# Kernel tuning notes

Hardware: AMD Instinct MI355X
Metric: run time of the kernel (lower is better)

## Reference

```python
import jax, jax.numpy as jnp
import numpy as np

N, HW, L = 16, 3136, 64
C_IN, C_OUT, D = 256, 512, 256


def setup_inputs() -> dict:
    key = jax.random.key(0)
    ks = jax.random.split(key, 8)
    # xavier-normal-ish scale for weights
    def xav(k, shape):
        fan_in, fan_out = shape[1], shape[0]
        std = (2.0 / (fan_in + fan_out)) ** 0.5
        return jax.random.normal(k, shape, dtype=jnp.float32) * std
    return {
        "x": jax.random.normal(ks[0], (N, HW, C_IN), dtype=jnp.float32),
        "t": jax.random.normal(ks[1], (N, L, D), dtype=jnp.float32),
        "W1": xav(ks[2], (D, C_IN)),      # linear1 weight (out,in), no bias
        "W2": xav(ks[3], (D, D)),         # linear2 weight, no bias
        "W3": xav(ks[4], (C_OUT, D)),     # linear3 weight
        "b3": jnp.zeros((C_OUT,), dtype=jnp.float32),
        "Wd": xav(ks[5], (C_OUT, C_IN)),  # downsample weight
        "bd": jnp.zeros((C_OUT,), dtype=jnp.float32),
    }


def reference(x, t, W1, W2, W3, b3, Wd, bd):
    # x: (N, HW, C_in), t: (N, L, D)
    x_q = jnp.einsum("npc,dc->npd", x, W1)          # (N, HW, D)
    t_q = jnp.einsum("nld,ed->nle", t, W2)          # (N, L, D)
    a = jnp.einsum("npd,nld->npl", x_q, t_q)        # unscaled QK^T (N, HW, L)
    a = jax.nn.softmax(a, axis=2)
    t3 = jnp.einsum("nld,od->nlo", t, W3) + b3      # (N, L, C_out)
    av = jnp.einsum("npl,nlo->npo", a, t3)          # (N, HW, C_out)
    x_ds = jnp.einsum("npc,oc->npo", x, Wd) + bd    # downsample residual
    return x_ds + av
```

## Files before the change

### kernel.cpp

```cpp
#include <hip/hip_runtime.h>


typedef unsigned short u16;
using half8 = __attribute__((ext_vector_type(8))) _Float16;
using f32x4 = __attribute__((ext_vector_type(4))) float;

__device__ __forceinline__ u16 f2h(float f) {
  _Float16 h = (_Float16)f;
  union { _Float16 h; u16 u; } cv; cv.h = h;
  return cv.u;
}

__device__ __forceinline__ f32x4 mfma16(half8 a, half8 b, f32x4 c) {
  return __builtin_amdgcn_mfma_f32_16x16x32_f16(a, b, c, 0, 0, 0);
}

__global__ __launch_bounds__(256) void reblock_kernel(
    const float* __restrict__ W1, const float* __restrict__ W2,
    const float* __restrict__ W3, const float* __restrict__ Wd,
    const float* __restrict__ t,
    u16* __restrict__ W1f, u16* __restrict__ W2f, u16* __restrict__ W3f,
    u16* __restrict__ Wdf, u16* __restrict__ tf) {
  int b = blockIdx.x, k = threadIdx.x;
  const float* src; u16* dst; int row;
  if (b < 256)       { src = W1; dst = W1f; row = b; }
  else if (b < 512)  { src = W2; dst = W2f; row = b - 256; }
  else if (b < 1024) { src = W3; dst = W3f; row = b - 512; }
  else if (b < 1536) { src = Wd; dst = Wdf; row = b - 1024; }
  else               { src = t;  dst = tf;  row = b - 1536; }
  float v = src[(size_t)row*256 + k];
  int flat = ((row >> 4)*8 + (k >> 5))*512 + ((k >> 3) & 3)*128 + (row & 15)*8 + (k & 7);
  dst[flat] = f2h(v);
}

__global__ __launch_bounds__(256) void tq_t3t_kernel(
    const u16* __restrict__ tf, const u16* __restrict__ W2f,
    const u16* __restrict__ W3f, const float* __restrict__ b3,
    u16* __restrict__ tqf, u16* __restrict__ t3f) {
  const int tid = threadIdx.x, w = tid >> 6, lane = tid & 63;
  const int quad = lane >> 4, l16 = lane & 15;
  const int b = blockIdx.x;

  if (b < 64) {
    const int n = b >> 2, eb = b & 3;
    const int gW2 = eb*4 + w;
    f32x4 acc[4];
    #pragma unroll
    for (int mt = 0; mt < 4; ++mt) acc[mt] = (f32x4){0.f, 0.f, 0.f, 0.f};
    #pragma unroll
    for (int kc = 0; kc < 8; ++kc) {
      half8 bf = *(const half8*)(W2f + (gW2*8 + kc)*512 + lane*8);
      #pragma unroll
      for (int mt = 0; mt < 4; ++mt) {
        half8 a = *(const half8*)(tf + ((n*4 + mt)*8 + kc)*512 + lane*8);
        acc[mt] = mfma16(a, bf, acc[mt]);
      }
    }
    #pragma unroll
    for (int mt = 0; mt < 4; ++mt)
      #pragma unroll
      for (int r = 0; r < 4; ++r) {
        int flat = ((n*4 + mt)*8 + eb*2 + (w >> 1))*512
                 + ((w & 1)*2 + (l16 >> 3))*128 + (quad*4 + r)*8 + (l16 & 7);
        tqf[flat] = f2h(acc[mt][r]);
      }
  } else {
    const int b2 = b - 64;
    const int n = b2 >> 3, ob = b2 & 7;
    const int gW3 = ob*4 + w;
    f32x4 acc[4];
    #pragma unroll
    for (int nt = 0; nt < 4; ++nt) acc[nt] = (f32x4){0.f, 0.f, 0.f, 0.f};
    #pragma unroll
    for (int kc = 0; kc < 8; ++kc) {
      half8 a = *(const half8*)(W3f + (gW3*8 + kc)*512 + lane*8);
      #pragma unroll
      for (int nt = 0; nt < 4; ++nt) {
        half8 bf = *(const half8*)(tf + ((n*4 + nt)*8 + kc)*512 + lane*8);
        acc[nt] = mfma16(a, bf, acc[nt]);
      }
    }
    #pragma unroll
    for (int nt = 0; nt < 4; ++nt)
      #pragma unroll
      for (int r = 0; r < 4; ++r) {
        int o = ob*64 + w*16 + quad*4 + r;
        int flat = ((n*32 + ob*4 + w)*2 + (nt >> 1))*512
                 + ((nt & 1)*2 + (l16 >> 3))*128 + (quad*4 + r)*8 + (l16 & 7);
        t3f[flat] = f2h(acc[nt][r] + b3[o]);
      }
  }
}

__global__ __launch_bounds__(512, 4) void main_kernel(
    const float* __restrict__ x, const u16* __restrict__ W1f,
    const u16* __restrict__ Wdf, const u16* __restrict__ tqf,
    const u16* __restrict__ t3f, const float* __restrict__ bd,
    float* __restrict__ out) {
  __shared__ u16 xs[64*264];
  __shared__ __align__(16) u16 pool[64*136];

  const int bid = blockIdx.x;
  const int n = bid / 49;
  const int pt = bid - n*49;
  const int m0 = pt * 64;
  const int tid = threadIdx.x, w = tid >> 6, lane = tid & 63;
  const int quad = lane >> 4, l16 = lane & 15;

  float bias[4];
  #pragma unroll
  for (int ot = 0; ot < 4; ++ot) bias[ot] = bd[w*64 + ot*16 + l16];

  {
    const float4* xg = (const float4*)(x + (size_t)(n*3136 + m0)*256);
    #pragma unroll
    for (int it = 0; it < 8; ++it) {
      int idx = it*512 + tid;
      int r = idx >> 6, c4 = idx & 63;
      float4 v = xg[idx];
      ushort4 u;
      u.x = f2h(v.x); u.y = f2h(v.y); u.z = f2h(v.z); u.w = f2h(v.w);
      *(ushort4*)(&xs[r*264 + c4*4]) = u;
    }
  }
  __syncthreads();

  f32x4 acc2[4];
  #pragma unroll
  for (int lt = 0; lt < 4; ++lt) acc2[lt] = (f32x4){0.f, 0.f, 0.f, 0.f};

  #pragma unroll
  for (int h = 0; h < 2; ++h) {
    f32x4 acc1[4];
    #pragma unroll
    for (int mt = 0; mt < 4; ++mt) acc1[mt] = (f32x4){0.f, 0.f, 0.f, 0.f};

    const u16* w1p = W1f + (h*8 + w)*8*512;
    #pragma unroll
    for (int kc = 0; kc < 8; ++kc) {
      half8 bf = *(const half8*)(w1p + kc*512 + lane*8);
      #pragma unroll
      for (int mt = 0; mt < 4; ++mt) {
        half8 a = *(const half8*)(&xs[(mt*16 + l16)*264 + kc*32 + quad*8]);
        acc1[mt] = mfma16(a, bf, acc1[mt]);
      }
    }
    __syncthreads();
    #pragma unroll
    for (int mt = 0; mt < 4; ++mt)
      #pragma unroll
      for (int r = 0; r < 4; ++r)
        pool[(mt*16 + quad*4 + r)*136 + w*16 + l16] = f2h(acc1[mt][r]);
    __syncthreads();

    if (w < 4) {
      #pragma unroll
      for (int k2 = 0; k2 < 4; ++k2) {
        half8 a = *(const half8*)(&pool[(w*16 + l16)*136 + k2*32 + quad*8]);
        #pragma unroll
        for (int lt = 0; lt < 4; ++lt) {
          half8 bf = *(const half8*)(tqf + ((n*4 + lt)*8 + h*4 + k2)*512 + lane*8);
          acc2[lt] = mfma16(a, bf, acc2[lt]);
        }
      }
    }
  }
  __syncthreads();

  if (w < 4) {
    #pragma unroll
    for (int r = 0; r < 4; ++r) {
      float s0 = acc2[0][r], s1 = acc2[1][r], s2 = acc2[2][r], s3 = acc2[3][r];
      float mx = fmaxf(fmaxf(s0, s1), fmaxf(s2, s3));
      #pragma unroll
      for (int off = 8; off >= 1; off >>= 1) mx = fmaxf(mx, __shfl_xor(mx, off, 64));
      float e0 = __expf(s0 - mx), e1 = __expf(s1 - mx);
      float e2 = __expf(s2 - mx), e3 = __expf(s3 - mx);
      float s = e0 + e1 + e2 + e3;
      #pragma unroll
      for (int off = 8; off >= 1; off >>= 1) s += __shfl_xor(s, off, 64);
      float inv = 1.0f / s;
      int row = (w*16 + quad*4 + r)*72;
      pool[row +  0 + l16] = f2h(e0 * inv);
      pool[row + 16 + l16] = f2h(e1 * inv);
      pool[row + 32 + l16] = f2h(e2 * inv);
      pool[row + 48 + l16] = f2h(e3 * inv);
    }
  }
  __syncthreads();

  f32x4 acc[4][4];
  #pragma unroll
  for (int mt = 0; mt < 4; ++mt)
    #pragma unroll
    for (int ot = 0; ot < 4; ++ot) acc[mt][ot] = (f32x4){0.f, 0.f, 0.f, 0.f};

  #pragma unroll
  for (int kc3 = 0; kc3 < 2; ++kc3) {
    half8 a[4];
    #pragma unroll
    for (int mt = 0; mt < 4; ++mt)
      a[mt] = *(const half8*)(&pool[(mt*16 + l16)*72 + kc3*32 + quad*8]);
    #pragma unroll
    for (int ot = 0; ot < 4; ++ot) {
      half8 bf = *(const half8*)(t3f + ((n*32 + w*4 + ot)*2 + kc3)*512 + lane*8);
      #pragma unroll
      for (int mt = 0; mt < 4; ++mt) acc[mt][ot] = mfma16(a[mt], bf, acc[mt][ot]);
    }
  }
  #pragma unroll
  for (int kc = 0; kc < 8; ++kc) {
    half8 a[4];
    #pragma unroll
    for (int mt = 0; mt < 4; ++mt)
      a[mt] = *(const half8*)(&xs[(mt*16 + l16)*264 + kc*32 + quad*8]);
    #pragma unroll
    for (int ot = 0; ot < 4; ++ot) {
      half8 bf = *(const half8*)(Wdf + ((w*4 + ot)*8 + kc)*512 + lane*8);
      #pragma unroll
      for (int mt = 0; mt < 4; ++mt) acc[mt][ot] = mfma16(a[mt], bf, acc[mt][ot]);
    }
  }
  __syncthreads();

  float* pf = (float*)pool;
  #pragma unroll
  for (int c = 0; c < 8; ++c) {
    int mt = c >> 1;
    if ((quad >> 1) == (c & 1)) {
      int rl = (quad & 1)*4;
      #pragma unroll
      for (int ot = 0; ot < 4; ++ot)
        #pragma unroll
        for (int r = 0; r < 4; ++r)
          pf[(rl + r)*520 + w*64 + ot*16 + l16] = acc[mt][ot][r] + bias[ot];
    }
    __syncthreads();
    #pragma unroll
    for (int j = 0; j < 2; ++j) {
      int flat = j*512 + tid;
      int rl = flat >> 7, c4 = (flat & 127)*4;
      float4 v = *(float4*)&pf[rl*520 + c4];
      *(float4*)&out[(size_t)(n*3136 + m0 + c*8 + rl)*512 + c4] = v;
    }
    __syncthreads();
  }
}

extern "C" void kernel_launch(void* const* d_in, const int* in_sizes, int n_in,
                              void* d_out, int out_size, void* d_ws, size_t ws_size,
                              hipStream_t stream) {
  const float* x  = (const float*)d_in[0];
  const float* t  = (const float*)d_in[1];
  const float* W1 = (const float*)d_in[2];
  const float* W2 = (const float*)d_in[3];
  const float* W3 = (const float*)d_in[4];
  const float* b3 = (const float*)d_in[5];
  const float* Wd = (const float*)d_in[6];
  const float* bd = (const float*)d_in[7];
  float* out = (float*)d_out;

  char* ws = (char*)d_ws;
  u16* W1f = (u16*)(ws + 0);
  u16* W2f = (u16*)(ws + 131072);
  u16* W3f = (u16*)(ws + 262144);
  u16* Wdf = (u16*)(ws + 524288);
  u16* tf  = (u16*)(ws + 786432);
  u16* tqf = (u16*)(ws + 1310720);
  u16* t3f = (u16*)(ws + 1835008);

  hipLaunchKernelGGL(reblock_kernel, dim3(2560), dim3(256), 0, stream,
                     W1, W2, W3, Wd, t, W1f, W2f, W3f, Wdf, tf);
  hipLaunchKernelGGL(tq_t3t_kernel, dim3(192), dim3(256), 0, stream,
                     tf, W2f, W3f, b3, tqf, t3f);
  hipLaunchKernelGGL(main_kernel, dim3(784), dim3(512), 0, stream,
                     x, W1f, Wdf, tqf, t3f, bd, out);
}
```

Before: 200.4 us.

## Overlap attention stages with downsample GEMM and use per-wave output staging

The fused kernel's schedule is reordered. W1 fragments for the first half are prefetched into registers before the x tile loads. The second-half x·W1 GEMM is interleaved with the first-half QK^T product, and the downsample GEMM now runs before the softmax barrier so its MFMAs can hide synchronisation latency. The epilogue replaces the block-wide eight-step staged store, which had two barriers per step, with a barrier-free per-wave staging area carved from a unified shared-memory buffer. The cost is higher register pressure from the prefetched W1 fragments and from the output accumulators staying live longer, which could limit occupancy.

New measurement: 196.8 us. Within noise of the previous version (-1.8%).

```diff
diff --git a/kernel.cpp b/kernel.cpp
--- a/kernel.cpp
+++ b/kernel.cpp
@@ -97,8 +97,9 @@
     const u16* __restrict__ Wdf, const u16* __restrict__ tqf,
     const u16* __restrict__ t3f, const float* __restrict__ bd,
     float* __restrict__ out) {
-  __shared__ u16 xs[64*264];
-  __shared__ __align__(16) u16 pool[64*136];
+  __shared__ __attribute__((aligned(16))) char smem[34816 + 17408];
+  u16* xs   = (u16*)smem;
+  u16* pool = (u16*)(smem + 34816);
 
   const int bid = blockIdx.x;
   const int n = bid / 49;
@@ -107,6 +108,12 @@
   const int tid = threadIdx.x, w = tid >> 6, lane = tid & 63;
   const int quad = lane >> 4, l16 = lane & 15;
 
+  half8 w1a[8];
+  {
+    const u16* p = W1f + (size_t)w*8*512;
+    #pragma unroll
+    for (int kc = 0; kc < 8; ++kc) w1a[kc] = *(const half8*)(p + kc*512 + lane*8);
+  }
   float bias[4];
   #pragma unroll
   for (int ot = 0; ot < 4; ++ot) bias[ot] = bd[w*64 + ot*16 + l16];
@@ -125,44 +132,88 @@
   }
   __syncthreads();
 
+  f32x4 acc1[4];
+  #pragma unroll
+  for (int mt = 0; mt < 4; ++mt) acc1[mt] = (f32x4){0.f, 0.f, 0.f, 0.f};
+  #pragma unroll
+  for (int kc = 0; kc < 8; ++kc)
+    #pragma unroll
+    for (int mt = 0; mt < 4; ++mt) {
+      half8 a = *(const half8*)(&xs[(mt*16 + l16)*264 + kc*32 + quad*8]);
+      acc1[mt] = mfma16(a, w1a[kc], acc1[mt]);
+    }
+  #pragma unroll
+  for (int mt = 0; mt < 4; ++mt)
+    #pragma unroll
+    for (int r = 0; r < 4; ++r)
+      pool[(mt*16 + quad*4 + r)*136 + w*16 + l16] = f2h(acc1[mt][r]);
+  __syncthreads();
+
   f32x4 acc2[4];
   #pragma unroll
   for (int lt = 0; lt < 4; ++lt) acc2[lt] = (f32x4){0.f, 0.f, 0.f, 0.f};
-
-  #pragma unroll
-  for (int h = 0; h < 2; ++h) {
-    f32x4 acc1[4];
-    #pragma unroll
-    for (int mt = 0; mt < 4; ++mt) acc1[mt] = (f32x4){0.f, 0.f, 0.f, 0.f};
-
-    const u16* w1p = W1f + (h*8 + w)*8*512;
+  f32x4 acc[4][4];
+  #pragma unroll
+  for (int mt = 0; mt < 4; ++mt)
+    #pragma unroll
+    for (int ot = 0; ot < 4; ++ot) acc[mt][ot] = (f32x4){0.f, 0.f, 0.f, 0.f};
+
+  f32x4 acc1b[4];
+  #pragma unroll
+  for (int mt = 0; mt < 4; ++mt) acc1b[mt] = (f32x4){0.f, 0.f, 0.f, 0.f};
+  {
+    const u16* p = W1f + (size_t)(8 + w)*8*512;
     #pragma unroll
     for (int kc = 0; kc < 8; ++kc) {
-      half8 bf = *(const half8*)(w1p + kc*512 + lane*8);
+      half8 bf = *(const half8*)(p + kc*512 + lane*8);
       #pragma unroll
       for (int mt = 0; mt < 4; ++mt) {
         half8 a = *(const half8*)(&xs[(mt*16 + l16)*264 + kc*32 + quad*8]);
-        acc1[mt] = mfma16(a, bf, acc1[mt]);
-      }
-    }
-    __syncthreads();
+        acc1b[mt] = mfma16(a, bf, acc1b[mt]);
+      }
+    }
+  }
+  if (w < 4) {
+    #pragma unroll
+    for (int k2 = 0; k2 < 4; ++k2) {
+      half8 a = *(const half8*)(&pool[(w*16 + l16)*136 + k2*32 + quad*8]);
+      #pragma unroll
+      for (int lt = 0; lt < 4; ++lt) {
+        half8 bf = *(const half8*)(tqf + ((n*4 + lt)*8 + 0*4 + k2)*512 + lane*8);
+        acc2[lt] = mfma16(a, bf, acc2[lt]);
+      }
+    }
+  }
+  __syncthreads();
+  #pragma unroll
+  for (int mt = 0; mt < 4; ++mt)
+    #pragma unroll
+    for (int r = 0; r < 4; ++r)
+      pool[(mt*16 + quad*4 + r)*136 + w*16 + l16] = f2h(acc1b[mt][r]);
+  __syncthreads();
+
+  if (w < 4) {
+    #pragma unroll
+    for (int k2 = 0; k2 < 4; ++k2) {
+      half8 a = *(const half8*)(&pool[(w*16 + l16)*136 + k2*32 + quad*8]);
+      #pragma unroll
+      for (int lt = 0; lt < 4; ++lt) {
+        half8 bf = *(const half8*)(tqf + ((n*4 + lt)*8 + 1*4 + k2)*512 + lane*8);
+        acc2[lt] = mfma16(a, bf, acc2[lt]);
+      }
+    }
+  }
+  #pragma unroll
+  for (int kc = 0; kc < 8; ++kc) {
+    half8 a[4];
     #pragma unroll
     for (int mt = 0; mt < 4; ++mt)
-      #pragma unroll
-      for (int r = 0; r < 4; ++r)
-        pool[(mt*16 + quad*4 + r)*136 + w*16 + l16] = f2h(acc1[mt][r]);
-    __syncthreads();
-
-    if (w < 4) {
-      #pragma unroll
-      for (int k2 = 0; k2 < 4; ++k2) {
-        half8 a = *(const half8*)(&pool[(w*16 + l16)*136 + k2*32 + quad*8]);
-        #pragma unroll
-        for (int lt = 0; lt < 4; ++lt) {
-          half8 bf = *(const half8*)(tqf + ((n*4 + lt)*8 + h*4 + k2)*512 + lane*8);
-          acc2[lt] = mfma16(a, bf, acc2[lt]);
-        }
-      }
+      a[mt] = *(const half8*)(&xs[(mt*16 + l16)*264 + kc*32 + quad*8]);
+    #pragma unroll
+    for (int ot = 0; ot < 4; ++ot) {
+      half8 bf = *(const half8*)(Wdf + ((w*4 + ot)*8 + kc)*512 + lane*8);
+      #pragma unroll
+      for (int mt = 0; mt < 4; ++mt) acc[mt][ot] = mfma16(a[mt], bf, acc[mt][ot]);
     }
   }
   __syncthreads();
@@ -189,12 +240,6 @@
   }
   __syncthreads();
 
-  f32x4 acc[4][4];
-  #pragma unroll
-  for (int mt = 0; mt < 4; ++mt)
-    #pragma unroll
-    for (int ot = 0; ot < 4; ++ot) acc[mt][ot] = (f32x4){0.f, 0.f, 0.f, 0.f};
-
   #pragma unroll
   for (int kc3 = 0; kc3 < 2; ++kc3) {
     half8 a[4];
@@ -208,42 +253,20 @@
       for (int mt = 0; mt < 4; ++mt) acc[mt][ot] = mfma16(a[mt], bf, acc[mt][ot]);
     }
   }
-  #pragma unroll
-  for (int kc = 0; kc < 8; ++kc) {
-    half8 a[4];
-    #pragma unroll
-    for (int mt = 0; mt < 4; ++mt)
-      a[mt] = *(const half8*)(&xs[(mt*16 + l16)*264 + kc*32 + quad*8]);
-    #pragma unroll
-    for (int ot = 0; ot < 4; ++ot) {
-      half8 bf = *(const half8*)(Wdf + ((w*4 + ot)*8 + kc)*512 + lane*8);
-      #pragma unroll
-      for (int mt = 0; mt < 4; ++mt) acc[mt][ot] = mfma16(a[mt], bf, acc[mt][ot]);
-    }
-  }
-  __syncthreads();
-
-  float* pf = (float*)pool;
-  #pragma unroll
-  for (int c = 0; c < 8; ++c) {
-    int mt = c >> 1;
-    if ((quad >> 1) == (c & 1)) {
-      int rl = (quad & 1)*4;
-      #pragma unroll
-      for (int ot = 0; ot < 4; ++ot)
-        #pragma unroll
-        for (int r = 0; r < 4; ++r)
-          pf[(rl + r)*520 + w*64 + ot*16 + l16] = acc[mt][ot][r] + bias[ot];
-    }
-    __syncthreads();
-    #pragma unroll
-    for (int j = 0; j < 2; ++j) {
-      int flat = j*512 + tid;
-      int rl = flat >> 7, c4 = (flat & 127)*4;
-      float4 v = *(float4*)&pf[rl*520 + c4];
-      *(float4*)&out[(size_t)(n*3136 + m0 + c*8 + rl)*512 + c4] = v;
-    }
-    __syncthreads();
+
+  float* sc = (float*)smem + w*1088;
+  #pragma unroll
+  for (int mt = 0; mt < 4; ++mt) {
+    #pragma unroll
+    for (int ot = 0; ot < 4; ++ot)
+      #pragma unroll
+      for (int r = 0; r < 4; ++r)
+        sc[(quad*4 + r)*68 + ot*16 + l16] = acc[mt][ot][r] + bias[ot];
+    #pragma unroll
+    for (int i = 0; i < 4; ++i) {
+      float4 v = *(float4*)&sc[(i*4 + quad)*68 + l16*4];
+      *(float4*)&out[(size_t)(n*3136 + m0 + mt*16 + i*4 + quad)*512 + w*64 + l16*4] = v;
+    }
   }
 }
 
```
